# Optimization experiments

Hardware: AMD Instinct MI355X
Metric: run time of the kernel (lower is better)

Reference implementation:

```python
import jax, jax.numpy as jnp
import numpy as np

BN_EPS = 1e-5  # torch BatchNorm1d default


def setup_inputs() -> dict:
    key = jax.random.key(0)
    ks = jax.random.split(key, 4)
    B, C, N, O = 8, 64, 4096, 64
    x = jax.random.normal(ks[0], (B, C, N, 1), dtype=jnp.float32)
    w1 = jax.random.normal(ks[1], (C, O), dtype=jnp.float32) * (1.0 / np.sqrt(C))
    b1 = jnp.zeros((O,), jnp.float32)
    gamma = jnp.ones((O,), jnp.float32)
    beta = jnp.zeros((O,), jnp.float32)
    w2 = jax.random.normal(ks[2], (O, O), dtype=jnp.float32) * (1.0 / np.sqrt(O))
    b2 = jnp.zeros((O,), jnp.float32)
    eps_gin = jnp.zeros((), jnp.float32)  # train_eps=True, init eps=0.0
    return {"x": x, "w1": w1, "b1": b1, "gamma": gamma, "beta": beta,
            "w2": w2, "b2": b2, "eps_gin": eps_gin, "k": 16}


def _knn_idx(xf, k):
    # xf: [B, N, C] -> indices of k nearest neighbors (incl. self, loop=True)
    sq = jnp.sum(xf * xf, axis=-1)                       # [B, N]
    d = sq[:, :, None] + sq[:, None, :] - 2.0 * jnp.einsum('bnc,bmc->bnm', xf, xf)
    _, idx = jax.lax.top_k(-d, k)                        # [B, N, k]
    return idx


def reference(x, w1, b1, gamma, beta, w2, b2, eps_gin, k):
    B, C, N, _ = x.shape
    xf = jnp.transpose(x[..., 0], (0, 2, 1))             # [B, N, C]
    idx = _knn_idx(xf, k)                                # [B, N, k]
    # GIN aggregation: each node has exactly k neighbors -> gather + sum
    gathered = jax.vmap(lambda xb, ib: xb[ib])(xf, idx)  # [B, N, k, C]
    aggr = gathered.sum(axis=2)                          # [B, N, C]
    h = (1.0 + eps_gin) * xf + aggr                      # [B, N, C]
    hf = h.reshape(B * N, C)
    h1 = hf @ w1 + b1                                    # [B*N, O]
    # BatchNorm1d, training-mode batch statistics (biased variance)
    mean = jnp.mean(h1, axis=0)
    var = jnp.mean((h1 - mean) ** 2, axis=0)
    hn = gamma * (h1 - mean) / jnp.sqrt(var + BN_EPS) + beta
    hg = jax.nn.gelu(hn, approximate=False)              # torch default GELU (erf)
    out = hg @ w2 + b2                                   # [B*N, O]
    return jnp.transpose(out.reshape(B, N, -1), (0, 2, 1))[..., None]  # [B, O, N, 1]
```

## Files before the change

### kernel.cpp

```cpp
#include <hip/hip_runtime.h>
#include <cstdint>
#include <cstddef>

#define B_ 8
#define C_ 64
#define N_ 4096
#define O_ 64
#define ROWS_ (B_*N_)
#define NSPLIT_ 2
#define CAPB_ 33
#define TAU_TILES_ 8
#define MIDROWS_ 16

typedef unsigned long long u64;
typedef unsigned int u32;
typedef unsigned short u16;
typedef __attribute__((ext_vector_type(8))) short bf16x8;
typedef __attribute__((ext_vector_type(16))) float f32x16;

#define MFMA32(A,Bv,Cv) __builtin_amdgcn_mfma_f32_32x32x16_bf16(A,Bv,Cv,0,0,0)

#define OFF_XF   0
#define OFF_SQ   8388608
#define OFF_KD   8519680
#define OFF_KI   16908288
#define OFF_PACK 21102592
#define OFF_H1   21102592
#define OFF_BN   33685504

__device__ __forceinline__ void insert16(u64 kv[16], u64 key) {
  if (key < kv[15]) {
#pragma unroll
    for (int j = 15; j > 0; --j) {
      u64 a = kv[j-1], b = kv[j];
      kv[j] = (key < a) ? a : ((key < b) ? key : b);
    }
    kv[0] = (key < kv[0]) ? key : kv[0];
  }
}

__global__ __launch_bounds__(256) void k_transpose(const float* __restrict__ x,
                                                   float* __restrict__ xf,
                                                   float* __restrict__ sq,
                                                   u16* __restrict__ pack) {
  __shared__ float lds[64 * 65];
  const int b  = blockIdx.x >> 6;
  const int n0 = (blockIdx.x & 63) << 6;
  const int tid = threadIdx.x;
  const float* xb = x + (size_t)b * C_ * N_;
  {
    const int nn = tid & 63;
    const int c0 = tid >> 6;
#pragma unroll
    for (int i = 0; i < 16; ++i) {
      int c = c0 + i * 4;
      lds[c * 65 + nn] = xb[(size_t)c * N_ + n0 + nn];
    }
  }
  __syncthreads();
  {
    const int cc  = tid & 63;
    const int nn0 = tid >> 6;
#pragma unroll
    for (int i = 0; i < 16; ++i) {
      int nn = nn0 + i * 4;
      xf[((size_t)(b * N_ + n0 + nn)) * 64 + cc] = lds[cc * 65 + nn];
    }
  }
  if (tid < 64) {
    float s = 0.f;
#pragma unroll
    for (int c = 0; c < 64; ++c) { float v = lds[c * 65 + tid]; s += v * v; }
    sq[b * N_ + n0 + tid] = s;
  }
  {
    const int lane = tid & 63;
    const int slice = tid >> 6;
    const int kb = slice * 16 + (lane >> 5) * 8;
#pragma unroll
    for (int tl = 0; tl < 2; ++tl) {
      const int nl = tl * 32 + (lane & 31);
      bf16x8 H, M, L;
#pragma unroll
      for (int j = 0; j < 8; ++j) {
        float f = lds[(kb + j) * 65 + nl];
        u32 u = __float_as_uint(f);
        u32 rh = (u + 0x7FFFu + ((u >> 16) & 1u)) >> 16;
        float bh = __uint_as_float(rh << 16);
        float f1 = f - bh;
        u = __float_as_uint(f1);
        u32 rm = (u + 0x7FFFu + ((u >> 16) & 1u)) >> 16;
        float bm = __uint_as_float(rm << 16);
        float f2 = f1 - bm;
        u = __float_as_uint(f2);
        u32 rl = (u + 0x7FFFu + ((u >> 16) & 1u)) >> 16;
        H[j] = (short)rh; M[j] = (short)rm; L[j] = (short)rl;
      }
      const int tile = ((blockIdx.x & 63) << 1) + tl;
      u16* basep = pack + ((size_t)(b * 128 + tile) * 12) * 512 + lane * 8;
      *(bf16x8*)(basep + (size_t)(0 + slice) * 512) = H;
      *(bf16x8*)(basep + (size_t)(4 + slice) * 512) = M;
      *(bf16x8*)(basep + (size_t)(8 + slice) * 512) = L;
    }
  }
}

#define KNN_LOAD(P, mt) do { const u16* ap_ = pb + (size_t)(mt) * (12*512); \
  P##h0 = *(const bf16x8*)(ap_ + 0*512);  P##h1 = *(const bf16x8*)(ap_ + 1*512); \
  P##h2 = *(const bf16x8*)(ap_ + 2*512);  P##h3 = *(const bf16x8*)(ap_ + 3*512); \
  P##m0 = *(const bf16x8*)(ap_ + 4*512);  P##m1 = *(const bf16x8*)(ap_ + 5*512); \
  P##m2 = *(const bf16x8*)(ap_ + 6*512);  P##m3 = *(const bf16x8*)(ap_ + 7*512); \
  P##l0 = *(const bf16x8*)(ap_ + 8*512);  P##l1 = *(const bf16x8*)(ap_ + 9*512); \
  P##l2 = *(const bf16x8*)(ap_ +10*512);  P##l3 = *(const bf16x8*)(ap_ +11*512); } while(0)

#define SQ_LOAD(MT) do { const float* sp_ = sqb + (MT) * 32 + 4 * h; \
  sv0 = *(const float4*)(sp_);      sv1 = *(const float4*)(sp_ + 8); \
  sv2 = *(const float4*)(sp_ + 16); sv3 = *(const float4*)(sp_ + 24); } while(0)

#define KNN_MFMA(P) \
  acc0 = MFMA32(P##h0, ql0, acc0);  acc1 = MFMA32(P##h1, ql1, acc1); \
  acc0 = MFMA32(P##l0, qh0, acc0);  acc1 = MFMA32(P##l1, qh1, acc1); \
  acc0 = MFMA32(P##m0, qm0, acc0);  acc1 = MFMA32(P##m1, qm1, acc1); \
  acc0 = MFMA32(P##h0, qm0, acc0);  acc1 = MFMA32(P##h1, qm1, acc1); \
  acc0 = MFMA32(P##m0, qh0, acc0);  acc1 = MFMA32(P##m1, qh1, acc1); \
  acc0 = MFMA32(P##h0, qh0, acc0);  acc1 = MFMA32(P##h1, qh1, acc1); \
  acc0 = MFMA32(P##h2, ql2, acc0);  acc1 = MFMA32(P##h3, ql3, acc1); \
  acc0 = MFMA32(P##l2, qh2, acc0);  acc1 = MFMA32(P##l3, qh3, acc1); \
  acc0 = MFMA32(P##m2, qm2, acc0);  acc1 = MFMA32(P##m3, qm3, acc1); \
  acc0 = MFMA32(P##h2, qm2, acc0);  acc1 = MFMA32(P##h3, qm3, acc1); \
  acc0 = MFMA32(P##m2, qh2, acc0);  acc1 = MFMA32(P##m3, qh3, acc1); \
  acc0 = MFMA32(P##h2, qh2, acc0);  acc1 = MFMA32(P##h3, qh3, acc1);

#define SEL_T8() do { \
  float sqv_[16] = {sv0.x, sv0.y, sv0.z, sv0.w, sv1.x, sv1.y, sv1.z, sv1.w, \
                    sv2.x, sv2.y, sv2.z, sv2.w, sv3.x, sv3.y, sv3.z, sv3.w}; \
_Pragma("unroll") \
  for (int r_ = 0; r_ < 16; ++r_) { \
    float d_ = fmaf(-2.f, acc0[r_] + acc1[r_], sqv_[r_]); \
    u32 u_ = __float_as_uint(d_); \
    u_ ^= ((int)u_ < 0) ? 0xFFFFFFFFu : 0x80000000u; \
    if (u_ < kv1[7]) { \
_Pragma("unroll") \
      for (int j_ = 7; j_ > 0; --j_) { \
        u32 a_ = kv1[j_-1], b_ = kv1[j_]; \
        kv1[j_] = (u_ < a_) ? a_ : ((u_ < b_) ? u_ : b_); \
      } \
      kv1[0] = (u_ < kv1[0]) ? u_ : kv1[0]; \
    } \
  } \
} while(0)

#define SEL_C(MT) do { \
  const u32 ic_ = (u32)((MT) * 32 + 4 * h); \
  float sqv_[16] = {sv0.x, sv0.y, sv0.z, sv0.w, sv1.x, sv1.y, sv1.z, sv1.w, \
                    sv2.x, sv2.y, sv2.z, sv2.w, sv3.x, sv3.y, sv3.z, sv3.w}; \
_Pragma("unroll") \
  for (int r_ = 0; r_ < 16; ++r_) { \
    float d_ = fmaf(-2.f, acc0[r_] + acc1[r_], sqv_[r_]); \
    u32 u_ = __float_as_uint(d_); \
    u_ ^= ((int)u_ < 0) ? 0xFFFFFFFFu : 0x80000000u; \
    if (u_ <= tauk) { \
      myc[cnt] = ((u64)u_ << 32) | (u64)(ic_ + (u32)((r_ & 3) + 8 * (r_ >> 2))); \
      ++cnt; \
    } \
  } \
  if (__any(cnt >= CAPB_ - 16)) {             \
    for (int i_ = 0; i_ < cnt; ++i_) insert16(kv, myc[i_]); \
    cnt = 0; \
  } \
} while(0)

__global__ __launch_bounds__(256, 2) void k_knn(const u16* __restrict__ pack,
                                                const float* __restrict__ sq,
                                                u32* __restrict__ kd,
                                                u16* __restrict__ ki,
                                                float* __restrict__ bn_acc) {
  __shared__ u64 cand[256 * CAPB_];
  const int bx = blockIdx.x;
  const int tid = threadIdx.x;
  if (bx == 0 && tid < 128) bn_acc[tid] = 0.f;
  const int split = bx & 1;
  const int qb = (bx >> 1) & 31;
  const int b = bx >> 6;
  const int lane = tid & 63;
  const int wid = tid >> 6;
  const int qt = qb * 4 + wid;
  const int h = lane >> 5;
  const u16* pb = pack + (size_t)b * (128 * 12 * 512) + lane * 8;

  const u16* qp = pb + (size_t)qt * (12 * 512);
  bf16x8 qh0 = *(const bf16x8*)(qp + 0*512), qh1 = *(const bf16x8*)(qp + 1*512);
  bf16x8 qh2 = *(const bf16x8*)(qp + 2*512), qh3 = *(const bf16x8*)(qp + 3*512);
  bf16x8 qm0 = *(const bf16x8*)(qp + 4*512), qm1 = *(const bf16x8*)(qp + 5*512);
  bf16x8 qm2 = *(const bf16x8*)(qp + 6*512), qm3 = *(const bf16x8*)(qp + 7*512);
  bf16x8 ql0 = *(const bf16x8*)(qp + 8*512), ql1 = *(const bf16x8*)(qp + 9*512);
  bf16x8 ql2 = *(const bf16x8*)(qp + 10*512), ql3 = *(const bf16x8*)(qp + 11*512);

  const float* sqb = sq + b * N_;
  const int mbase = split * 64;

  bf16x8 Ah0, Ah1, Ah2, Ah3, Am0, Am1, Am2, Am3, Al0, Al1, Al2, Al3;
  bf16x8 Bh0, Bh1, Bh2, Bh3, Bm0, Bm1, Bm2, Bm3, Bl0, Bl1, Bl2, Bl3;
  float4 sv0, sv1, sv2, sv3;

  u32 kv1[8];
#pragma unroll
  for (int j = 0; j < 8; ++j) kv1[j] = 0xFF800000u;

  KNN_LOAD(A, mbase);
  for (int ct = 0; ct < TAU_TILES_; ct += 2) {
    SQ_LOAD(mbase + ct);
    KNN_LOAD(B, mbase + ct + 1);
    {
      f32x16 acc0 = {0,0,0,0,0,0,0,0,0,0,0,0,0,0,0,0};
      f32x16 acc1 = {0,0,0,0,0,0,0,0,0,0,0,0,0,0,0,0};
      KNN_MFMA(A)
      SEL_T8();
    }
    SQ_LOAD(mbase + ct + 1);
    KNN_LOAD(A, mbase + ct + 2);
    {
      f32x16 acc0 = {0,0,0,0,0,0,0,0,0,0,0,0,0,0,0,0};
      f32x16 acc1 = {0,0,0,0,0,0,0,0,0,0,0,0,0,0,0,0};
      KNN_MFMA(B)
      SEL_T8();
    }
  }
  u32 tk = kv1[7];
  u32 pk = (u32)__shfl_xor((int)tk, 32);
  const u32 tauk = (tk > pk) ? tk : pk;

  u64 kv[16];
#pragma unroll
  for (int j = 0; j < 16; ++j) kv[j] = 0xFF8000000000FFFFull;
  int cnt = 0;
  u64* myc = cand + tid * CAPB_;

  KNN_LOAD(A, mbase);
  for (int ct = 0; ct < 64; ct += 2) {
    SQ_LOAD(mbase + ct);
    KNN_LOAD(B, mbase + ct + 1);
    {
      f32x16 acc0 = {0,0,0,0,0,0,0,0,0,0,0,0,0,0,0,0};
      f32x16 acc1 = {0,0,0,0,0,0,0,0,0,0,0,0,0,0,0,0};
      KNN_MFMA(A)
      SEL_C(mbase + ct);
    }
    SQ_LOAD(mbase + ct + 1);
    KNN_LOAD(A, mbase + ((ct + 2) & 63));
    {
      f32x16 acc0 = {0,0,0,0,0,0,0,0,0,0,0,0,0,0,0,0};
      f32x16 acc1 = {0,0,0,0,0,0,0,0,0,0,0,0,0,0,0,0};
      KNN_MFMA(B)
      SEL_C(mbase + ct + 1);
    }
  }
  for (int i = 0; i < cnt; ++i) insert16(kv, myc[i]);

  u64 m[16];
#pragma unroll
  for (int j = 0; j < 16; ++j) {
    u64 p = __shfl_xor(kv[15 - j], 32);
    m[j] = (kv[j] < p) ? kv[j] : p;
  }
#pragma unroll
  for (int d = 8; d >= 1; d >>= 1) {
#pragma unroll
    for (int j = 0; j < 16; ++j) {
      if ((j & d) == 0) {
        u64 a = m[j], c = m[j | d];
        m[j] = (a < c) ? a : c;
        m[j | d] = (a < c) ? c : a;
      }
    }
  }

  if (lane < 32) {
    const int row = b * N_ + qt * 32 + lane;
    u32* dp = kd + ((size_t)row * NSPLIT_ + split) * 16;
    u16* ip = ki + ((size_t)row * NSPLIT_ + split) * 16;
#pragma unroll
    for (int j = 0; j < 16; ++j) {
      dp[j] = (u32)(m[j] >> 32);
      ip[j] = (u16)(m[j] & 0xFFFFu);
    }
  }
}

__global__ __launch_bounds__(256) void k_mid(const u32* __restrict__ kd,
                                             const u16* __restrict__ ki,
                                             const float* __restrict__ xf,
                                             const float* __restrict__ eps_gin,
                                             const float* __restrict__ w1,
                                             const float* __restrict__ b1,
                                             float* __restrict__ h1,
                                             float* __restrict__ bn_acc) {
  __shared__ float wT[64 * 65];
  __shared__ float hL[MIDROWS_ * 65];
  __shared__ int   knnL[MIDROWS_ * 16];
  __shared__ float rs[4][64], rs2[4][64];
  const int tid = threadIdx.x;
  const int r0 = blockIdx.x * MIDROWS_;
#pragma unroll
  for (int i = 0; i < 16; ++i) {
    int idx = tid + i * 256;
    wT[(idx & 63) * 65 + (idx >> 6)] = w1[idx];
  }
  {
    const int row = tid >> 4;
    const int j = tid & 15;
    const u32* dp = kd + (size_t)(r0 + row) * (NSPLIT_ * 16);
    const u16* ip = ki + (size_t)(r0 + row) * (NSPLIT_ * 16);
    u64 a = ((u64)dp[j] << 32) | ip[j];
    u64 bb = ((u64)dp[16 + (15 - j)] << 32) | ip[16 + (15 - j)];
    knnL[row * 16 + j] = (int)((a < bb ? a : bb) & 0xFFFFu);
  }
  __syncthreads();
  const int c = tid & 63;
  const int q = tid >> 6;
  const int b = r0 >> 12;
  const float* xfb = xf + (size_t)b * N_ * 64;
  const float eps1 = 1.f + eps_gin[0];
#pragma unroll
  for (int i = 0; i < 4; ++i) {
    int rl = q * 4 + i;
    float v = eps1 * xfb[(size_t)((r0 & (N_ - 1)) + rl) * 64 + c];
    const int* kn = knnL + rl * 16;
#pragma unroll
    for (int j = 0; j < 16; ++j) {
      int mr = kn[j];
      v += xfb[(size_t)mr * 64 + c];
    }
    hL[rl * 65 + c] = v;
  }
  __syncthreads();
  const int o = c;
  const float bias = b1[o];
  float s = 0.f, s2 = 0.f;
#pragma unroll
  for (int i = 0; i < 4; ++i) {
    int rl = q * 4 + i;
    float acc = bias;
#pragma unroll
    for (int k = 0; k < 16; ++k) {
      float4 hv = *(const float4*)&hL[rl * 65 + 4 * k];
      float4 wv = *(const float4*)&wT[o * 65 + 4 * k];
      acc += hv.x * wv.x; acc += hv.y * wv.y;
      acc += hv.z * wv.z; acc += hv.w * wv.w;
    }
    h1[(size_t)(r0 + rl) * 64 + o] = acc;
    s += acc; s2 += acc * acc;
  }
  rs[q][o] = s; rs2[q][o] = s2;
  __syncthreads();
  if (tid < 64) {
    float ts  = rs[0][tid] + rs[1][tid] + rs[2][tid] + rs[3][tid];
    float ts2 = rs2[0][tid] + rs2[1][tid] + rs2[2][tid] + rs2[3][tid];
    atomicAdd(&bn_acc[tid], ts);
    atomicAdd(&bn_acc[64 + tid], ts2);
  }
}

__global__ __launch_bounds__(256) void k_final(const float* __restrict__ h1,
                                               const float* __restrict__ bn_acc,
                                               const float* __restrict__ gamma,
                                               const float* __restrict__ beta,
                                               const float* __restrict__ w2,
                                               const float* __restrict__ b2,
                                               float* __restrict__ out) {
  __shared__ float wT2[64 * 65];
  __shared__ float hg[64 * 65];
  __shared__ float scsh[128];
  const int tid = threadIdx.x;
#pragma unroll
  for (int i = 0; i < 16; ++i) {
    int idx = tid + i * 256;
    wT2[(idx & 63) * 65 + (idx >> 6)] = w2[idx];
  }
  if (tid < 64) {
    const float inv = 1.f / (float)ROWS_;
    float mean = bn_acc[tid] * inv;
    float var  = bn_acc[64 + tid] * inv - mean * mean;
    float sc = gamma[tid] * rsqrtf(var + 1e-5f);
    scsh[tid] = sc;
    scsh[64 + tid] = beta[tid] - mean * sc;
  }
  __syncthreads();
  const int r0 = blockIdx.x * 64;
  const int b  = r0 >> 12;
  const int n0 = r0 & (N_ - 1);
  const int o = tid & 63;
  const int q = tid >> 6;
  const float sc = scsh[o], sh = scsh[64 + o];
#pragma unroll
  for (int i = 0; i < 16; ++i) {
    int rl = q + i * 4;
    float v = h1[(size_t)(r0 + rl) * 64 + o] * sc + sh;
    float g = 0.5f * v * (1.f + erff(v * 0.70710678118654752f));
    hg[rl * 65 + o] = g;
  }
  __syncthreads();
  const int nl = tid & 63;
  float4 hv[16];
#pragma unroll
  for (int k = 0; k < 16; ++k) hv[k] = *(const float4*)&hg[nl * 65 + 4 * k];
#pragma unroll
  for (int i = 0; i < 16; ++i) {
    int o2 = q + i * 4;
    float acc = b2[o2];
#pragma unroll
    for (int k = 0; k < 16; ++k) {
      float4 wv = *(const float4*)&wT2[o2 * 65 + 4 * k];
      acc += hv[k].x * wv.x; acc += hv[k].y * wv.y;
      acc += hv[k].z * wv.z; acc += hv[k].w * wv.w;
    }
    out[((size_t)(b * 64 + o2)) * N_ + n0 + nl] = acc;
  }
}

extern "C" void kernel_launch(void* const* d_in, const int* in_sizes, int n_in,
                              void* d_out, int out_size, void* d_ws, size_t ws_size,
                              hipStream_t stream) {
  const float* x     = (const float*)d_in[0];
  const float* w1    = (const float*)d_in[1];
  const float* b1    = (const float*)d_in[2];
  const float* gamma = (const float*)d_in[3];
  const float* beta  = (const float*)d_in[4];
  const float* w2    = (const float*)d_in[5];
  const float* b2    = (const float*)d_in[6];
  const float* eps_g = (const float*)d_in[7];
  float* out = (float*)d_out;

  char* ws = (char*)d_ws;
  float* xf   = (float*)(ws + OFF_XF);
  float* sq   = (float*)(ws + OFF_SQ);
  u32*   kd   = (u32*)  (ws + OFF_KD);
  u16*   ki   = (u16*)  (ws + OFF_KI);
  u16*   pack = (u16*)  (ws + OFF_PACK);
  float* h1   = (float*)(ws + OFF_H1);
  float* bn_acc = (float*)(ws + OFF_BN);

  k_transpose<<<512, 256, 0, stream>>>(x, xf, sq, pack);
  k_knn<<<512, 256, 0, stream>>>(pack, sq, kd, ki, bn_acc);
  k_mid<<<ROWS_ / MIDROWS_, 256, 0, stream>>>(kd, ki, xf, eps_g, w1, b1, h1, bn_acc);
  k_final<<<ROWS_ / 64, 256, 0, stream>>>(h1, bn_acc, gamma, beta, w2, b2, out);
}
```

Before: 333.9 us.

## Split KNN into producer/consumer wave pairs passing distance tiles through LDS

Reorganizes the KNN kernel so each query tile is handled by a pair of waves: one computes MFMA distance tiles and writes them to a double-buffered LDS area, and the other reads them and performs the top-k threshold and candidate selection. The intent is to overlap matrix-core work with the scalar selection logic, which were previously serialized within one wave. The grid doubles to 1024 blocks with half the queries per block, and a block-wide barrier is taken every step. Risks include barrier overhead, load imbalance between producer and consumer work, and half the waves doing only MFMA.

```diff
diff --git a/kernel.cpp b/kernel.cpp
--- a/kernel.cpp
+++ b/kernel.cpp
@@ -113,10 +113,6 @@
   P##l0 = *(const bf16x8*)(ap_ + 8*512);  P##l1 = *(const bf16x8*)(ap_ + 9*512); \
   P##l2 = *(const bf16x8*)(ap_ +10*512);  P##l3 = *(const bf16x8*)(ap_ +11*512); } while(0)
 
-#define SQ_LOAD(MT) do { const float* sp_ = sqb + (MT) * 32 + 4 * h; \
-  sv0 = *(const float4*)(sp_);      sv1 = *(const float4*)(sp_ + 8); \
-  sv2 = *(const float4*)(sp_ + 16); sv3 = *(const float4*)(sp_ + 24); } while(0)
-
 #define KNN_MFMA(P) \
   acc0 = MFMA32(P##h0, ql0, acc0);  acc1 = MFMA32(P##h1, ql1, acc1); \
   acc0 = MFMA32(P##l0, qh0, acc0);  acc1 = MFMA32(P##l1, qh1, acc1); \
@@ -131,12 +127,18 @@
   acc0 = MFMA32(P##m2, qh2, acc0);  acc1 = MFMA32(P##m3, qh3, acc1); \
   acc0 = MFMA32(P##h2, qh2, acc0);  acc1 = MFMA32(P##h3, qh3, acc1);
 
+#define SQ_LOADN(MT) do { const float* sp_ = sqb + (MT) * 32 + 4 * h; \
+  svn0 = *(const float4*)(sp_);      svn1 = *(const float4*)(sp_ + 8); \
+  svn2 = *(const float4*)(sp_ + 16); svn3 = *(const float4*)(sp_ + 24); } while(0)
+
 #define SEL_T8() do { \
-  float sqv_[16] = {sv0.x, sv0.y, sv0.z, sv0.w, sv1.x, sv1.y, sv1.z, sv1.w, \
-                    sv2.x, sv2.y, sv2.z, sv2.w, sv3.x, sv3.y, sv3.z, sv3.w}; \
+  float sqv_[16] = {svc0.x, svc0.y, svc0.z, svc0.w, svc1.x, svc1.y, svc1.z, svc1.w, \
+                    svc2.x, svc2.y, svc2.z, svc2.w, svc3.x, svc3.y, svc3.z, svc3.w}; \
+  float dd_[16]  = {dv0.x, dv0.y, dv0.z, dv0.w, dv1.x, dv1.y, dv1.z, dv1.w, \
+                    dv2.x, dv2.y, dv2.z, dv2.w, dv3.x, dv3.y, dv3.z, dv3.w}; \
 _Pragma("unroll") \
   for (int r_ = 0; r_ < 16; ++r_) { \
-    float d_ = fmaf(-2.f, acc0[r_] + acc1[r_], sqv_[r_]); \
+    float d_ = fmaf(-2.f, dd_[r_], sqv_[r_]); \
     u32 u_ = __float_as_uint(d_); \
     u_ ^= ((int)u_ < 0) ? 0xFFFFFFFFu : 0x80000000u; \
     if (u_ < kv1[7]) { \
@@ -152,11 +154,13 @@
 
 #define SEL_C(MT) do { \
   const u32 ic_ = (u32)((MT) * 32 + 4 * h); \
-  float sqv_[16] = {sv0.x, sv0.y, sv0.z, sv0.w, sv1.x, sv1.y, sv1.z, sv1.w, \
-                    sv2.x, sv2.y, sv2.z, sv2.w, sv3.x, sv3.y, sv3.z, sv3.w}; \
+  float sqv_[16] = {svc0.x, svc0.y, svc0.z, svc0.w, svc1.x, svc1.y, svc1.z, svc1.w, \
+                    svc2.x, svc2.y, svc2.z, svc2.w, svc3.x, svc3.y, svc3.z, svc3.w}; \
+  float dd_[16]  = {dv0.x, dv0.y, dv0.z, dv0.w, dv1.x, dv1.y, dv1.z, dv1.w, \
+                    dv2.x, dv2.y, dv2.z, dv2.w, dv3.x, dv3.y, dv3.z, dv3.w}; \
 _Pragma("unroll") \
   for (int r_ = 0; r_ < 16; ++r_) { \
-    float d_ = fmaf(-2.f, acc0[r_] + acc1[r_], sqv_[r_]); \
+    float d_ = fmaf(-2.f, dd_[r_], sqv_[r_]); \
     u32 u_ = __float_as_uint(d_); \
     u_ ^= ((int)u_ < 0) ? 0xFFFFFFFFu : 0x80000000u; \
     if (u_ <= tauk) { \
@@ -175,114 +179,136 @@
                                                 u32* __restrict__ kd,
                                                 u16* __restrict__ ki,
                                                 float* __restrict__ bn_acc) {
-  __shared__ u64 cand[256 * CAPB_];
+  __shared__ float dist[2 * 2 * 64 * 16];
+  __shared__ u64 cand[128 * CAPB_];
   const int bx = blockIdx.x;
   const int tid = threadIdx.x;
   if (bx == 0 && tid < 128) bn_acc[tid] = 0.f;
   const int split = bx & 1;
-  const int qb = (bx >> 1) & 31;
-  const int b = bx >> 6;
+  const int qp = (bx >> 1) & 63;
+  const int b = bx >> 7;
   const int lane = tid & 63;
   const int wid = tid >> 6;
-  const int qt = qb * 4 + wid;
+  const int pair = wid >> 1;
+  const bool prod = ((wid ^ bx) & 1) == 0;
+  const int qt = qp * 2 + pair;
   const int h = lane >> 5;
   const u16* pb = pack + (size_t)b * (128 * 12 * 512) + lane * 8;
-
-  const u16* qp = pb + (size_t)qt * (12 * 512);
-  bf16x8 qh0 = *(const bf16x8*)(qp + 0*512), qh1 = *(const bf16x8*)(qp + 1*512);
-  bf16x8 qh2 = *(const bf16x8*)(qp + 2*512), qh3 = *(const bf16x8*)(qp + 3*512);
-  bf16x8 qm0 = *(const bf16x8*)(qp + 4*512), qm1 = *(const bf16x8*)(qp + 5*512);
-  bf16x8 qm2 = *(const bf16x8*)(qp + 6*512), qm3 = *(const bf16x8*)(qp + 7*512);
-  bf16x8 ql0 = *(const bf16x8*)(qp + 8*512), ql1 = *(const bf16x8*)(qp + 9*512);
-  bf16x8 ql2 = *(const bf16x8*)(qp + 10*512), ql3 = *(const bf16x8*)(qp + 11*512);
-
   const float* sqb = sq + b * N_;
   const int mbase = split * 64;
 
+  bf16x8 qh0, qh1, qh2, qh3, qm0, qm1, qm2, qm3, ql0, ql1, ql2, ql3;
+  if (prod) {
+    const u16* qp_ = pb + (size_t)qt * (12 * 512);
+    qh0 = *(const bf16x8*)(qp_ + 0*512);  qh1 = *(const bf16x8*)(qp_ + 1*512);
+    qh2 = *(const bf16x8*)(qp_ + 2*512);  qh3 = *(const bf16x8*)(qp_ + 3*512);
+    qm0 = *(const bf16x8*)(qp_ + 4*512);  qm1 = *(const bf16x8*)(qp_ + 5*512);
+    qm2 = *(const bf16x8*)(qp_ + 6*512);  qm3 = *(const bf16x8*)(qp_ + 7*512);
+    ql0 = *(const bf16x8*)(qp_ + 8*512);  ql1 = *(const bf16x8*)(qp_ + 9*512);
+    ql2 = *(const bf16x8*)(qp_ + 10*512); ql3 = *(const bf16x8*)(qp_ + 11*512);
+  }
   bf16x8 Ah0, Ah1, Ah2, Ah3, Am0, Am1, Am2, Am3, Al0, Al1, Al2, Al3;
-  bf16x8 Bh0, Bh1, Bh2, Bh3, Bm0, Bm1, Bm2, Bm3, Bl0, Bl1, Bl2, Bl3;
-  float4 sv0, sv1, sv2, sv3;
 
   u32 kv1[8];
-#pragma unroll
-  for (int j = 0; j < 8; ++j) kv1[j] = 0xFF800000u;
-
-  KNN_LOAD(A, mbase);
-  for (int ct = 0; ct < TAU_TILES_; ct += 2) {
-    SQ_LOAD(mbase + ct);
-    KNN_LOAD(B, mbase + ct + 1);
-    {
-      f32x16 acc0 = {0,0,0,0,0,0,0,0,0,0,0,0,0,0,0,0};
-      f32x16 acc1 = {0,0,0,0,0,0,0,0,0,0,0,0,0,0,0,0};
-      KNN_MFMA(A)
-      SEL_T8();
-    }
-    SQ_LOAD(mbase + ct + 1);
-    KNN_LOAD(A, mbase + ct + 2);
-    {
-      f32x16 acc0 = {0,0,0,0,0,0,0,0,0,0,0,0,0,0,0,0};
-      f32x16 acc1 = {0,0,0,0,0,0,0,0,0,0,0,0,0,0,0,0};
-      KNN_MFMA(B)
-      SEL_T8();
-    }
-  }
-  u32 tk = kv1[7];
-  u32 pk = (u32)__shfl_xor((int)tk, 32);
-  const u32 tauk = (tk > pk) ? tk : pk;
-
   u64 kv[16];
-#pragma unroll
-  for (int j = 0; j < 16; ++j) kv[j] = 0xFF8000000000FFFFull;
+  u32 tauk = 0;
   int cnt = 0;
-  u64* myc = cand + tid * CAPB_;
-
-  KNN_LOAD(A, mbase);
-  for (int ct = 0; ct < 64; ct += 2) {
-    SQ_LOAD(mbase + ct);
-    KNN_LOAD(B, mbase + ct + 1);
-    {
-      f32x16 acc0 = {0,0,0,0,0,0,0,0,0,0,0,0,0,0,0,0};
-      f32x16 acc1 = {0,0,0,0,0,0,0,0,0,0,0,0,0,0,0,0};
-      KNN_MFMA(A)
-      SEL_C(mbase + ct);
-    }
-    SQ_LOAD(mbase + ct + 1);
-    KNN_LOAD(A, mbase + ((ct + 2) & 63));
-    {
-      f32x16 acc0 = {0,0,0,0,0,0,0,0,0,0,0,0,0,0,0,0};
-      f32x16 acc1 = {0,0,0,0,0,0,0,0,0,0,0,0,0,0,0,0};
-      KNN_MFMA(B)
-      SEL_C(mbase + ct + 1);
-    }
-  }
-  for (int i = 0; i < cnt; ++i) insert16(kv, myc[i]);
-
-  u64 m[16];
-#pragma unroll
-  for (int j = 0; j < 16; ++j) {
-    u64 p = __shfl_xor(kv[15 - j], 32);
-    m[j] = (kv[j] < p) ? kv[j] : p;
-  }
-#pragma unroll
-  for (int d = 8; d >= 1; d >>= 1) {
+  u64* myc = cand + (size_t)(pair * 64 + lane) * CAPB_;
+  float4 svc0, svc1, svc2, svc3, svn0, svn1, svn2, svn3;
+  float4 dv0, dv1, dv2, dv3;
+  if (!prod) {
+#pragma unroll
+    for (int j = 0; j < 8; ++j) kv1[j] = 0xFF800000u;
+    const float* sp_ = sqb + mbase * 32 + 4 * h;
+    svc0 = *(const float4*)(sp_);      svc1 = *(const float4*)(sp_ + 8);
+    svc2 = *(const float4*)(sp_ + 16); svc3 = *(const float4*)(sp_ + 24);
+  }
+
+#pragma unroll 1
+  for (int s = 0; s < 73; ++s) {
+    if (prod) {
+      if (s < 72) {
+        const int mt = mbase + (s < TAU_TILES_ ? s : s - TAU_TILES_);
+        KNN_LOAD(A, mt);
+        f32x16 acc0 = {0,0,0,0,0,0,0,0,0,0,0,0,0,0,0,0};
+        f32x16 acc1 = {0,0,0,0,0,0,0,0,0,0,0,0,0,0,0,0};
+        KNN_MFMA(A)
+        float* wp = dist + ((size_t)(pair * 2 + (s & 1)) * 64 + lane) * 16;
+        float4 w;
+        w.x = acc0[0]  + acc1[0];  w.y = acc0[1]  + acc1[1];
+        w.z = acc0[2]  + acc1[2];  w.w = acc0[3]  + acc1[3];
+        *(float4*)(wp) = w;
+        w.x = acc0[4]  + acc1[4];  w.y = acc0[5]  + acc1[5];
+        w.z = acc0[6]  + acc1[6];  w.w = acc0[7]  + acc1[7];
+        *(float4*)(wp + 4) = w;
+        w.x = acc0[8]  + acc1[8];  w.y = acc0[9]  + acc1[9];
+        w.z = acc0[10] + acc1[10]; w.w = acc0[11] + acc1[11];
+        *(float4*)(wp + 8) = w;
+        w.x = acc0[12] + acc1[12]; w.y = acc0[13] + acc1[13];
+        w.z = acc0[14] + acc1[14]; w.w = acc0[15] + acc1[15];
+        *(float4*)(wp + 12) = w;
+      }
+    } else {
+      if (s >= 1) {
+        const int t = s - 1;
+        const int mt = mbase + (t < TAU_TILES_ ? t : t - TAU_TILES_);
+        const int tn = t + 1;
+        const int mtn = mbase + (tn < TAU_TILES_ ? tn : ((tn - TAU_TILES_) & 63));
+        SQ_LOADN(mtn);
+        const float* dpd = dist + ((size_t)(pair * 2 + ((s - 1) & 1)) * 64 + lane) * 16;
+        dv0 = *(const float4*)(dpd);
+        dv1 = *(const float4*)(dpd + 4);
+        dv2 = *(const float4*)(dpd + 8);
+        dv3 = *(const float4*)(dpd + 12);
+        if (t < TAU_TILES_) {
+          SEL_T8();
+        } else {
+          if (t == TAU_TILES_) {
+            u32 tk = kv1[7];
+            u32 pk = (u32)__shfl_xor((int)tk, 32);
+            tauk = (tk > pk) ? tk : pk;
+#pragma unroll
+            for (int j = 0; j < 16; ++j) kv[j] = 0xFF8000000000FFFFull;
+            cnt = 0;
+          }
+          SEL_C(mt);
+        }
+        svc0 = svn0; svc1 = svn1; svc2 = svn2; svc3 = svn3;
+      }
+    }
+    __syncthreads();
+  }
+
+  if (!prod) {
+    for (int i = 0; i < cnt; ++i) insert16(kv, myc[i]);
+
+    u64 m[16];
 #pragma unroll
     for (int j = 0; j < 16; ++j) {
-      if ((j & d) == 0) {
-        u64 a = m[j], c = m[j | d];
-        m[j] = (a < c) ? a : c;
-        m[j | d] = (a < c) ? c : a;
+      u64 p = __shfl_xor(kv[15 - j], 32);
+      m[j] = (kv[j] < p) ? kv[j] : p;
+    }
+#pragma unroll
+    for (int d = 8; d >= 1; d >>= 1) {
+#pragma unroll
+      for (int j = 0; j < 16; ++j) {
+        if ((j & d) == 0) {
+          u64 a = m[j], c = m[j | d];
+          m[j] = (a < c) ? a : c;
+          m[j | d] = (a < c) ? c : a;
+        }
       }
     }
-  }
-
-  if (lane < 32) {
-    const int row = b * N_ + qt * 32 + lane;
-    u32* dp = kd + ((size_t)row * NSPLIT_ + split) * 16;
-    u16* ip = ki + ((size_t)row * NSPLIT_ + split) * 16;
-#pragma unroll
-    for (int j = 0; j < 16; ++j) {
-      dp[j] = (u32)(m[j] >> 32);
-      ip[j] = (u16)(m[j] & 0xFFFFu);
+
+    if (lane < 32) {
+      const int row = b * N_ + qt * 32 + lane;
+      u32* dp = kd + ((size_t)row * NSPLIT_ + split) * 16;
+      u16* ip = ki + ((size_t)row * NSPLIT_ + split) * 16;
+#pragma unroll
+      for (int j = 0; j < 16; ++j) {
+        dp[j] = (u32)(m[j] >> 32);
+        ip[j] = (u16)(m[j] & 0xFFFFu);
+      }
     }
   }
 }
@@ -441,7 +467,7 @@
   float* bn_acc = (float*)(ws + OFF_BN);
 
   k_transpose<<<512, 256, 0, stream>>>(x, xf, sq, pack);
-  k_knn<<<512, 256, 0, stream>>>(pack, sq, kd, ki, bn_acc);
+  k_knn<<<1024, 256, 0, stream>>>(pack, sq, kd, ki, bn_acc);
   k_mid<<<ROWS_ / MIDROWS_, 256, 0, stream>>>(kd, ki, xf, eps_g, w1, b1, h1, bn_acc);
   k_final<<<ROWS_ / 64, 256, 0, stream>>>(h1, bn_acc, gamma, beta, w2, b2, out);
 }
```

New measurement: 536.4 us. 1.61x slower.
